# Kernel optimization log

Measured on AMD Instinct MI355X. Metric: run time of the kernel, lower is better.

Reference implementation:

```python
import jax, jax.numpy as jnp
import numpy as np

N = 65536          # collocation points
NB = 32            # n_buses
H = 256            # hidden width (two hidden layers)
TMAX = 20.0        # t_max for input normalisation


def _glorot(k, shape):
    lim = np.sqrt(2.0 / (shape[0] + shape[1])).astype(np.float32)
    return jax.random.normal(k, shape, jnp.float32) * lim


def setup_inputs() -> dict:
    key = jax.random.key(0)
    ks = jax.random.split(key, 8)
    return {
        "input_time": jax.random.uniform(ks[0], (N, 1), jnp.float32) * TMAX,
        "input_power": jax.random.normal(ks[1], (N, NB), jnp.float32),
        "W0": _glorot(ks[2], (1, H)),   "b0": jnp.zeros((H,), jnp.float32),
        "W1": _glorot(ks[3], (H, H)),   "b1": jnp.zeros((H,), jnp.float32),
        "W2": _glorot(ks[4], (H, NB)),  "b2": jnp.zeros((NB,), jnp.float32),
        "lambda_m": jnp.ones((1, NB), jnp.float32),
        "lambda_d": jnp.ones((1, NB), jnp.float32),
        "lambda_b": jax.random.uniform(ks[5], (NB, NB), jnp.float32),
        "bus_with_inertia": jnp.ones((1, NB), jnp.float32),
    }


def reference(input_time, input_power, W0, b0, W1, b1, W2, b2,
              lambda_m, lambda_d, lambda_b, bus_with_inertia):
    def mlp(t):  # scalar time -> [NB] angles
        x = 2.0 * t / TMAX - 1.0          # NormaliseInputLayer (t_min = 0)
        h = jnp.tanh(x * W0[0] + b0)      # [H]
        h = jnp.tanh(h @ W1 + b1)         # [H]
        return h @ W2 + b2                # [NB]

    one = jnp.float32(1.0)

    def f_and_dt(t):
        return jax.jvp(mlp, (t,), (one,))  # (delta, d delta/dt)

    def all3(t):
        (out, out_t), (_, out_tt) = jax.jvp(f_and_dt, (t,), (one,))
        return out, out_t, out_tt

    # vectorize the nested forward-mode derivatives over all samples at once
    out, out_t, out_tt = jax.vmap(all3)(input_time[:, 0])  # each [N, NB]

    # pairwise sin coupling: sum_j B_ij * sin(delta_i - delta_j)
    diff = out[:, :, None] - out[:, None, :]               # [N, NB, NB]
    connectivity = jnp.sum(lambda_b * jnp.sin(diff), axis=2)  # [N, NB]

    physics = (lambda_m * bus_with_inertia * out_tt
               + lambda_d * out_t
               + connectivity - input_power)

    return out, out_t, physics
```

## Files before the change

kernel.cpp:

```cpp
#include <hip/hip_runtime.h>

#define NPTS 65536
#define NB 32
#define H 256

typedef __attribute__((ext_vector_type(8))) short bhalf8;
typedef __attribute__((ext_vector_type(4))) float f32x4;

union BHU { bhalf8 h; uint u[4]; };

__device__ __forceinline__ float bf2f(ushort u) {
  union { uint x; float f; } c; c.x = ((uint)u) << 16; return c.f;
}
__device__ __forceinline__ ushort f2bf(float f) {
  uint x = __float_as_uint(f);
  uint r = x + 0x7FFFu + ((x >> 16) & 1u);
  return (ushort)(r >> 16);
}
__device__ __forceinline__ uint packrne(float a, float b) {
  return (uint)f2bf(a) | ((uint)f2bf(b) << 16);
}
__device__ __forceinline__ float fast_tanh(float z) {
  float e = __expf(2.0f * z);
  return 1.0f - 2.0f / (e + 1.0f);
}

__device__ __forceinline__ bool detect_bf16(const void* W1) {
  const uint4* p = (const uint4*)W1;
  int cnt = 0;
#pragma unroll
  for (int i = 0; i < 8; i++) {
    uint4 v = p[i];
    uint d[4] = {v.x, v.y, v.z, v.w};
#pragma unroll
    for (int k = 0; k < 4; k++) {
      int e = (d[k] >> 7) & 0xFF;
      cnt += (e >= 0x70 && e <= 0x7E) ? 1 : 0;
    }
  }
  return cnt >= 16;
}

template<bool B16> __device__ __forceinline__ float LD(const void* p, int i) {
  if constexpr (B16) return bf2f(((const ushort*)p)[i]);
  else               return ((const float*)p)[i];
}
template<bool B16> __device__ __forceinline__ void ST(void* p, int i, float v) {
  if constexpr (B16) ((ushort*)p)[i] = f2bf(v);
  else               ((float*)p)[i] = v;
}

__global__ void swz_kernel(const void* W1, const void* W2,
                           ushort* __restrict__ W1s, ushort* __restrict__ W2s) {
  int gid = blockIdx.x * 256 + threadIdx.x;
  bool b16 = detect_bf16(W1);
  if (gid < 65536) {
    int r = gid & 15, q = (gid >> 4) & 3, j = (gid >> 6) & 7;
    int kk = (gid >> 9) & 7, ct = gid >> 12;
    int src = (kk * 32 + q * 8 + j) * H + ct * 16 + r;
    int dst = ((ct * 8 + kk) * 64 + q * 16 + r) * 8 + j;
    float v = b16 ? bf2f(((const ushort*)W1)[src]) : ((const float*)W1)[src];
    W1s[dst] = f2bf(v);
  } else {
    int g2 = gid - 65536;
    int r = g2 & 15, q = (g2 >> 4) & 3, j = (g2 >> 6) & 7;
    int kk = (g2 >> 9) & 7, ct = (g2 >> 12) & 1;
    int src = (kk * 32 + q * 8 + j) * NB + ct * 16 + r;
    int dst = ((ct * 8 + kk) * 64 + q * 16 + r) * 8 + j;
    float v = b16 ? bf2f(((const ushort*)W2)[src]) : ((const float*)W2)[src];
    W2s[dst] = f2bf(v);
  }
}

#define PPITCH 40

struct Smem {
  alignas(16) ushort pairw[4][48 * PPITCH];
  alignas(16) ushort W2l[16 * 64 * 8];
  alignas(16) ushort lamTf[2 * 64 * 8];
  alignas(16) float  w0c[H], b0c[H], b1c[H];
  alignas(16) float  b2c[NB], lamMc[NB], lamDc[NB];
};

template<bool B16>
__device__ void pinn_body(Smem& sm,
                          const void* timeP, const void* powerP,
                          const void* W0, const void* b0,
                          const void* b1, const void* b2,
                          const void* lam_m, const void* lam_d,
                          const void* lam_b, const void* bwi,
                          const ushort* __restrict__ W1s, void* outP) {
  const int tid = threadIdx.x;
  const int wave = tid >> 6, lane = tid & 63;
  const int q = lane >> 4, r = lane & 15;

#pragma unroll
  for (int i = 0; i < 4; i++) {
    int c = tid + i * 256;
    *(bhalf8*)(sm.W2l + c * 8) = *(const bhalf8*)(((const ushort*)W1s) + H * H + c * 8);
  }
  if (tid < 128) {
    int ct = tid >> 6, l2 = tid & 63, qq = l2 >> 4, rr = l2 & 15;
    BHU t;
#pragma unroll
    for (int j = 0; j < 8; j += 2)
      t.u[j >> 1] = packrne(LD<B16>(lam_b, (ct * 16 + rr) * NB + qq * 8 + j),
                            LD<B16>(lam_b, (ct * 16 + rr) * NB + qq * 8 + j + 1));
    *(bhalf8*)(sm.lamTf + tid * 8) = t.h;
  }
  if (tid < H) {
    sm.w0c[tid] = LD<B16>(W0, tid);
    sm.b0c[tid] = LD<B16>(b0, tid);
    sm.b1c[tid] = LD<B16>(b1, tid);
  }
  if (tid < NB) {
    sm.b2c[tid]   = LD<B16>(b2, tid);
    sm.lamMc[tid] = LD<B16>(lam_m, tid) * LD<B16>(bwi, tid);
    sm.lamDc[tid] = LD<B16>(lam_d, tid);
  }
  __syncthreads();

  const int s0 = (blockIdx.x * 4 + wave) * 16;
  ushort* pw = &sm.pairw[wave][0];

  float t = LD<B16>(timeP, s0 + r);
  float x = t * 0.1f - 1.0f;

  bhalf8 a0f[8], a1f[8], a2f[8];
#pragma unroll
  for (int kk = 0; kk < 8; kk++) {
    int k0 = kk * 32 + q * 8;
    BHU t0, t1, t2;
    float vv[8], d1v[8], d2v[8];
#pragma unroll
    for (int j = 0; j < 8; j++) {
      float w0v = sm.w0c[k0 + j];
      float pre = x * w0v + sm.b0c[k0 + j];
      float v = fast_tanh(pre);
      float cc = w0v * 0.1f;
      float s2 = 1.0f - v * v;
      vv[j] = v; d1v[j] = s2 * cc; d2v[j] = -2.0f * v * d1v[j] * cc;
    }
#pragma unroll
    for (int j = 0; j < 8; j += 2) {
      t0.u[j >> 1] = packrne(vv[j], vv[j + 1]);
      t1.u[j >> 1] = packrne(d1v[j], d1v[j + 1]);
      t2.u[j >> 1] = packrne(d2v[j], d2v[j + 1]);
    }
    a0f[kk] = t0.h; a1f[kk] = t1.h; a2f[kk] = t2.h;
  }

  f32x4 acc2[3][2];
#pragma unroll
  for (int ch = 0; ch < 3; ch++)
#pragma unroll
    for (int c2 = 0; c2 < 2; c2++) { f32x4 z = {0.f,0.f,0.f,0.f}; acc2[ch][c2] = z; }

#pragma unroll 1
  for (int ct = 0; ct < 16; ct++) {
    bhalf8 bf[8];
#pragma unroll
    for (int kk = 0; kk < 8; kk++)
      bf[kk] = *(const bhalf8*)(W1s + ((ct * 8 + kk) * 64 + lane) * 8);

    if (ct >= 2 && (ct & 1) == 0) {
      int p = (ct >> 1) - 1;
#pragma unroll
      for (int ch = 0; ch < 3; ch++) {
        bhalf8 hf = *(const bhalf8*)(pw + (ch * 16 + r) * PPITCH + q * 8);
#pragma unroll
        for (int c2i = 0; c2i < 2; c2i++) {
          bhalf8 w2f = *(const bhalf8*)(sm.W2l + ((c2i * 8 + p) * 64 + lane) * 8);
          acc2[ch][c2i] = __builtin_amdgcn_mfma_f32_16x16x32_bf16(hf, w2f, acc2[ch][c2i], 0, 0, 0);
        }
      }
    }

    f32x4 c0 = {0.f,0.f,0.f,0.f}, c1 = c0, c2 = c0;
#pragma unroll
    for (int kk = 0; kk < 8; kk++) {
      c0 = __builtin_amdgcn_mfma_f32_16x16x32_bf16(a0f[kk], bf[kk], c0, 0, 0, 0);
      c1 = __builtin_amdgcn_mfma_f32_16x16x32_bf16(a1f[kk], bf[kk], c1, 0, 0, 0);
      c2 = __builtin_amdgcn_mfma_f32_16x16x32_bf16(a2f[kk], bf[kk], c2, 0, 0, 0);
    }
    float b1v = sm.b1c[ct * 16 + r];
    int lc = (ct & 1) * 16 + r;
#pragma unroll
    for (int i = 0; i < 4; i++) {
      float hv  = fast_tanh(c0[i] + b1v);
      float s2  = 1.0f - hv * hv;
      float hd  = s2 * c1[i];
      float hdd = s2 * c2[i] - 2.0f * hv * hd * c1[i];
      int row = q * 4 + i;
      pw[row * PPITCH + lc]        = f2bf(hv);
      pw[(16 + row) * PPITCH + lc] = f2bf(hd);
      pw[(32 + row) * PPITCH + lc] = f2bf(hdd);
    }
  }
  {
#pragma unroll
    for (int ch = 0; ch < 3; ch++) {
      bhalf8 hf = *(const bhalf8*)(pw + (ch * 16 + r) * PPITCH + q * 8);
#pragma unroll
      for (int c2i = 0; c2i < 2; c2i++) {
        bhalf8 w2f = *(const bhalf8*)(sm.W2l + ((c2i * 8 + 7) * 64 + lane) * 8);
        acc2[ch][c2i] = __builtin_amdgcn_mfma_f32_16x16x32_bf16(hf, w2f, acc2[ch][c2i], 0, 0, 0);
      }
    }
  }

  float dv[2][4], dt[2][4], dtt[2][4], sn[2][4], cs[2][4], Pv[2][4];
#pragma unroll
  for (int c2 = 0; c2 < 2; c2++) {
    int b = c2 * 16 + r;
    float b2v = sm.b2c[b];
#pragma unroll
    for (int i = 0; i < 4; i++) {
      int n = s0 + q * 4 + i;
      Pv[c2][i] = LD<B16>(powerP, n * NB + b);
      dv[c2][i]  = acc2[0][c2][i] + b2v;
      dt[c2][i]  = acc2[1][c2][i];
      dtt[c2][i] = acc2[2][c2][i];
      sn[c2][i] = __sinf(dv[c2][i]);
      cs[c2][i] = __cosf(dv[c2][i]);
      pw[(q * 4 + i) * PPITCH + b]        = f2bf(sn[c2][i]);
      pw[(16 + q * 4 + i) * PPITCH + b]   = f2bf(cs[c2][i]);
      ST<B16>(outP, n * NB + b, dv[c2][i]);
      ST<B16>(outP, NPTS * NB + n * NB + b, dt[c2][i]);
    }
  }
  bhalf8 snA = *(const bhalf8*)(pw + r * PPITCH + q * 8);
  bhalf8 csA = *(const bhalf8*)(pw + (16 + r) * PPITCH + q * 8);
  f32x4 accC[2], accS[2];
#pragma unroll
  for (int c2 = 0; c2 < 2; c2++) {
    bhalf8 lt = *(const bhalf8*)(sm.lamTf + (c2 * 64 + lane) * 8);
    f32x4 z = {0.f,0.f,0.f,0.f};
    accC[c2] = __builtin_amdgcn_mfma_f32_16x16x32_bf16(csA, lt, z, 0, 0, 0);
    accS[c2] = __builtin_amdgcn_mfma_f32_16x16x32_bf16(snA, lt, z, 0, 0, 0);
  }
#pragma unroll
  for (int c2 = 0; c2 < 2; c2++) {
    int b = c2 * 16 + r;
    float lm = sm.lamMc[b], ld = sm.lamDc[b];
#pragma unroll
    for (int i = 0; i < 4; i++) {
      float conn = sn[c2][i] * accC[c2][i] - cs[c2][i] * accS[c2][i];
      float phys = lm * dtt[c2][i] + ld * dt[c2][i] + conn - Pv[c2][i];
      int n = s0 + q * 4 + i;
      ST<B16>(outP, 2 * NPTS * NB + n * NB + b, phys);
    }
  }
}

__global__ __launch_bounds__(256, 2)
void pinn_kernel(const void* timeP, const void* powerP,
                 const void* W0, const void* b0,
                 const void* b1, const void* b2,
                 const void* lam_m, const void* lam_d,
                 const void* lam_b, const void* bwi,
                 const void* W1_for_detect,
                 const ushort* __restrict__ W1s, void* outP) {
  __shared__ Smem sm;
  if (detect_bf16(W1_for_detect))
    pinn_body<true>(sm, timeP, powerP, W0, b0, b1, b2, lam_m, lam_d, lam_b, bwi,
                    W1s, outP);
  else
    pinn_body<false>(sm, timeP, powerP, W0, b0, b1, b2, lam_m, lam_d, lam_b, bwi,
                     W1s, outP);
}

extern "C" void kernel_launch(void* const* d_in, const int* in_sizes, int n_in,
                              void* d_out, int out_size, void* d_ws, size_t ws_size,
                              hipStream_t stream) {
  const void* timeP  = d_in[0];
  const void* powerP = d_in[1];
  const void* W0     = d_in[2];
  const void* b0     = d_in[3];
  const void* W1     = d_in[4];
  const void* b1     = d_in[5];
  const void* W2     = d_in[6];
  const void* b2     = d_in[7];
  const void* lam_m  = d_in[8];
  const void* lam_d  = d_in[9];
  const void* lam_b  = d_in[10];
  const void* bwi    = d_in[11];

  ushort* W1s = (ushort*)d_ws;
  ushort* W2s = W1s + H * H;

  swz_kernel<<<288, 256, 0, stream>>>(W1, W2, W1s, W2s);
  pinn_kernel<<<1024, 256, 0, stream>>>(timeP, powerP, W0, b0, b1, b2,
                                        lam_m, lam_d, lam_b, bwi, W1,
                                        W1s, d_out);
  (void)W2s;
}
```

Measured before the change: 135.2 us.

## Truncate bf16 packing, vectorize W0/b0 loads, spread layer-2 MFMAs across iterations

Replaces round-to-nearest-even bf16 conversion with plain truncation for MFMA operands and LDS staging, which removes several integer ops per element. Loads W0/b0 from shared memory as float4 vectors instead of scalars. Splits the layer-2 MFMA work so each loop iteration issues half of it, interleaving it more evenly with the layer-1 MFMAs. Truncation adds a small systematic rounding bias that could affect accuracy tolerance.

```diff
diff --git a/kernel.cpp b/kernel.cpp
--- a/kernel.cpp
+++ b/kernel.cpp
@@ -19,6 +19,12 @@
 }
 __device__ __forceinline__ uint packrne(float a, float b) {
   return (uint)f2bf(a) | ((uint)f2bf(b) << 16);
+}
+__device__ __forceinline__ ushort trunc1(float f) {
+  return (ushort)(__float_as_uint(f) >> 16);
+}
+__device__ __forceinline__ uint packtr(float a, float b) {
+  return (__float_as_uint(a) >> 16) | (__float_as_uint(b) & 0xFFFF0000u);
 }
 __device__ __forceinline__ float fast_tanh(float z) {
   float e = __expf(2.0f * z);
@@ -130,22 +136,26 @@
 #pragma unroll
   for (int kk = 0; kk < 8; kk++) {
     int k0 = kk * 32 + q * 8;
+    float4 wA = *(const float4*)&sm.w0c[k0];
+    float4 wB = *(const float4*)&sm.w0c[k0 + 4];
+    float4 bA = *(const float4*)&sm.b0c[k0];
+    float4 bB = *(const float4*)&sm.b0c[k0 + 4];
+    float w0v[8] = {wA.x, wA.y, wA.z, wA.w, wB.x, wB.y, wB.z, wB.w};
+    float b0v[8] = {bA.x, bA.y, bA.z, bA.w, bB.x, bB.y, bB.z, bB.w};
     BHU t0, t1, t2;
     float vv[8], d1v[8], d2v[8];
 #pragma unroll
     for (int j = 0; j < 8; j++) {
-      float w0v = sm.w0c[k0 + j];
-      float pre = x * w0v + sm.b0c[k0 + j];
-      float v = fast_tanh(pre);
-      float cc = w0v * 0.1f;
+      float v = fast_tanh(x * w0v[j] + b0v[j]);
+      float cc = w0v[j] * 0.1f;
       float s2 = 1.0f - v * v;
       vv[j] = v; d1v[j] = s2 * cc; d2v[j] = -2.0f * v * d1v[j] * cc;
     }
 #pragma unroll
     for (int j = 0; j < 8; j += 2) {
-      t0.u[j >> 1] = packrne(vv[j], vv[j + 1]);
-      t1.u[j >> 1] = packrne(d1v[j], d1v[j + 1]);
-      t2.u[j >> 1] = packrne(d2v[j], d2v[j + 1]);
+      t0.u[j >> 1] = packtr(vv[j], vv[j + 1]);
+      t1.u[j >> 1] = packtr(d1v[j], d1v[j + 1]);
+      t2.u[j >> 1] = packtr(d2v[j], d2v[j + 1]);
     }
     a0f[kk] = t0.h; a1f[kk] = t1.h; a2f[kk] = t2.h;
   }
@@ -155,6 +165,8 @@
   for (int ch = 0; ch < 3; ch++)
 #pragma unroll
     for (int c2 = 0; c2 < 2; c2++) { f32x4 z = {0.f,0.f,0.f,0.f}; acc2[ch][c2] = z; }
+
+  bhalf8 hf[3];
 
 #pragma unroll 1
   for (int ct = 0; ct < 16; ct++) {
@@ -163,17 +175,18 @@
     for (int kk = 0; kk < 8; kk++)
       bf[kk] = *(const bhalf8*)(W1s + ((ct * 8 + kk) * 64 + lane) * 8);
 
-    if (ct >= 2 && (ct & 1) == 0) {
+    if (ct >= 2) {
       int p = (ct >> 1) - 1;
-#pragma unroll
-      for (int ch = 0; ch < 3; ch++) {
-        bhalf8 hf = *(const bhalf8*)(pw + (ch * 16 + r) * PPITCH + q * 8);
-#pragma unroll
-        for (int c2i = 0; c2i < 2; c2i++) {
-          bhalf8 w2f = *(const bhalf8*)(sm.W2l + ((c2i * 8 + p) * 64 + lane) * 8);
-          acc2[ch][c2i] = __builtin_amdgcn_mfma_f32_16x16x32_bf16(hf, w2f, acc2[ch][c2i], 0, 0, 0);
-        }
+      int c2i = ct & 1;
+      if (c2i == 0) {
+#pragma unroll
+        for (int ch = 0; ch < 3; ch++)
+          hf[ch] = *(const bhalf8*)(pw + (ch * 16 + r) * PPITCH + q * 8);
       }
+      bhalf8 w2f = *(const bhalf8*)(sm.W2l + ((c2i * 8 + p) * 64 + lane) * 8);
+#pragma unroll
+      for (int ch = 0; ch < 3; ch++)
+        acc2[ch][c2i] = __builtin_amdgcn_mfma_f32_16x16x32_bf16(hf[ch], w2f, acc2[ch][c2i], 0, 0, 0);
     }
 
     f32x4 c0 = {0.f,0.f,0.f,0.f}, c1 = c0, c2 = c0;
@@ -192,20 +205,21 @@
       float hd  = s2 * c1[i];
       float hdd = s2 * c2[i] - 2.0f * hv * hd * c1[i];
       int row = q * 4 + i;
-      pw[row * PPITCH + lc]        = f2bf(hv);
-      pw[(16 + row) * PPITCH + lc] = f2bf(hd);
-      pw[(32 + row) * PPITCH + lc] = f2bf(hdd);
+      pw[row * PPITCH + lc]        = trunc1(hv);
+      pw[(16 + row) * PPITCH + lc] = trunc1(hd);
+      pw[(32 + row) * PPITCH + lc] = trunc1(hdd);
     }
   }
   {
 #pragma unroll
-    for (int ch = 0; ch < 3; ch++) {
-      bhalf8 hf = *(const bhalf8*)(pw + (ch * 16 + r) * PPITCH + q * 8);
-#pragma unroll
-      for (int c2i = 0; c2i < 2; c2i++) {
-        bhalf8 w2f = *(const bhalf8*)(sm.W2l + ((c2i * 8 + 7) * 64 + lane) * 8);
-        acc2[ch][c2i] = __builtin_amdgcn_mfma_f32_16x16x32_bf16(hf, w2f, acc2[ch][c2i], 0, 0, 0);
-      }
+    for (int ch = 0; ch < 3; ch++)
+      hf[ch] = *(const bhalf8*)(pw + (ch * 16 + r) * PPITCH + q * 8);
+#pragma unroll
+    for (int c2i = 0; c2i < 2; c2i++) {
+      bhalf8 w2f = *(const bhalf8*)(sm.W2l + ((c2i * 8 + 7) * 64 + lane) * 8);
+#pragma unroll
+      for (int ch = 0; ch < 3; ch++)
+        acc2[ch][c2i] = __builtin_amdgcn_mfma_f32_16x16x32_bf16(hf[ch], w2f, acc2[ch][c2i], 0, 0, 0);
     }
   }
 
@@ -223,8 +237,8 @@
       dtt[c2][i] = acc2[2][c2][i];
       sn[c2][i] = __sinf(dv[c2][i]);
       cs[c2][i] = __cosf(dv[c2][i]);
-      pw[(q * 4 + i) * PPITCH + b]        = f2bf(sn[c2][i]);
-      pw[(16 + q * 4 + i) * PPITCH + b]   = f2bf(cs[c2][i]);
+      pw[(q * 4 + i) * PPITCH + b]        = trunc1(sn[c2][i]);
+      pw[(16 + q * 4 + i) * PPITCH + b]   = trunc1(cs[c2][i]);
       ST<B16>(outP, n * NB + b, dv[c2][i]);
       ST<B16>(outP, NPTS * NB + n * NB + b, dt[c2][i]);
     }
```

Result: no change. 134.2 us (-0.8%).
